# Optimization experiments

Hardware: AMD Instinct MI355X
Metric: run time of the kernel (lower is better)

## Reference

```python
import jax, jax.numpy as jnp
import numpy as np


def frame_align(x, R):
    # x: (..., N, d), R: (..., N, d, d)
    x = x - x.mean(axis=-2, keepdims=True)
    # R_inv = R^T applied per frame l to every point k: out[..., l, k, i]
    return jnp.einsum('...lji,...kj->...lki', R, x)


def setup_inputs() -> dict:
    key = jax.random.key(0)
    k1, k2, k3, k4 = jax.random.split(key, 4)
    B, N, d = 4, 2048, 3
    x = jax.random.normal(k1, (B, N, d), dtype=jnp.float32)
    R_x = jax.random.normal(k2, (B, N, d, d), dtype=jnp.float32)
    y = jax.random.normal(k3, (B, N, d), dtype=jnp.float32)
    R_y = jax.random.normal(k4, (B, N, d, d), dtype=jnp.float32)
    return {"x": x, "R_x": R_x, "y": y, "R_y": R_y}


def reference(x, R_x, y, R_y):
    x_aligned = frame_align(x, R_x)  # (B, N, N, d)
    y_aligned = frame_align(y, R_y)  # (B, N, N, d)
    return jnp.mean((x_aligned - y_aligned) ** 2)
```

## Files before the change

kernel.cpp:

```cpp
#include <hip/hip_runtime.h>

#define BATCH 4
#define NPTS  2048
#define TPB   256
#define BPB   8
#define NBLK  (BATCH * BPB)
#define NACC  48


__device__ float g_partial[NBLK][NACC];
__device__ int   g_ticket = 0;

__global__ __launch_bounds__(TPB)
void fape_single_kernel(const float* __restrict__ x,
                        const float* __restrict__ Rx,
                        const float* __restrict__ y,
                        const float* __restrict__ Ry,
                        float* __restrict__ out)
{
    const int blk = blockIdx.x;
    const int b   = blk >> 3;
    const int kb  = blk & 7;
    const int tid = threadIdx.x;
    const int n   = kb * TPB + tid;

    const float* __restrict__ xb  = x  + (size_t)b * NPTS * 3 + (size_t)n * 3;
    const float* __restrict__ yb  = y  + (size_t)b * NPTS * 3 + (size_t)n * 3;
    const float* __restrict__ rxb = Rx + (size_t)b * NPTS * 9 + (size_t)n * 9;
    const float* __restrict__ ryb = Ry + (size_t)b * NPTS * 9 + (size_t)n * 9;

    const int pi[6] = {0, 1, 2, 0, 0, 1};
    const int pj[6] = {0, 1, 2, 1, 2, 2};

    float xv[3], yv[3], rx[9], ry[9];
#pragma unroll
    for (int i = 0; i < 3; ++i) { xv[i] = xb[i]; yv[i] = yb[i]; }
#pragma unroll
    for (int i = 0; i < 9; ++i) { rx[i] = rxb[i]; ry[i] = ryb[i]; }

    float acc[NACC];
#pragma unroll
    for (int i = 0; i < 3; ++i) { acc[i] = xv[i]; acc[3 + i] = yv[i]; }
#pragma unroll
    for (int p = 0; p < 6; ++p) {
        const int i = pi[p], j = pj[p];
        acc[6  + p] = xv[i] * xv[j];
        acc[12 + p] = yv[i] * yv[j];
        float a = 0.f, bb = 0.f;
#pragma unroll
        for (int m = 0; m < 3; ++m) {
            a  += rx[i * 3 + m] * rx[j * 3 + m];
            bb += ry[i * 3 + m] * ry[j * 3 + m];
        }
        acc[27 + p] = a;
        acc[33 + p] = bb;
    }
#pragma unroll
    for (int i = 0; i < 3; ++i) {
#pragma unroll
        for (int j = 0; j < 3; ++j) {
            acc[18 + i * 3 + j] = xv[i] * yv[j];
            float c = 0.f;
#pragma unroll
            for (int m = 0; m < 3; ++m) c += rx[i * 3 + m] * ry[j * 3 + m];
            acc[39 + i * 3 + j] = c;
        }
    }

#pragma unroll
    for (int off = 32; off > 0; off >>= 1) {
#pragma unroll
        for (int q = 0; q < NACC; ++q) acc[q] += __shfl_down(acc[q], off, 64);
    }

    __shared__ float red[TPB / 64][NACC];
    const int wave = tid >> 6, lane = tid & 63;
    if (lane == 0) {
#pragma unroll
        for (int q = 0; q < NACC; ++q) red[wave][q] = acc[q];
    }
    __syncthreads();

    if (tid < NACC) {
        g_partial[blk][tid] = red[0][tid] + red[1][tid] + red[2][tid] + red[3][tid];
    }
    __threadfence();
    __syncthreads();

    __shared__ int slast;
    if (tid == 0) {
        const int old = atomicAdd(&g_ticket, 1);
        slast = (old == NBLK - 1);
    }
    __syncthreads();
    if (!slast) return;

    __threadfence();
    volatile const float* vp = &g_partial[0][0];

    __shared__ float fin[BATCH][NACC];
    if (tid < BATCH * NACC) {
        const int bb = tid / NACC, q = tid % NACC;
        float s = 0.f;
#pragma unroll
        for (int k = 0; k < BPB; ++k) s += vp[(bb * BPB + k) * NACC + q];
        fin[bb][q] = s;
    }
    __syncthreads();

    __shared__ double dots[BATCH];
    if (tid < BATCH) {
        const float* f = fin[tid];
        const double Ninv = 1.0 / (double)NPTS;
        double sx[3], sy[3];
        for (int i = 0; i < 3; ++i) { sx[i] = f[0 + i]; sy[i] = f[3 + i]; }

        double Sx[6], Sy[6], Sxy[9];
        for (int p = 0; p < 6; ++p) {
            const int i = pi[p], j = pj[p];
            Sx[p] = (double)f[6  + p] - sx[i] * sx[j] * Ninv;
            Sy[p] = (double)f[12 + p] - sy[i] * sy[j] * Ninv;
        }
        for (int i = 0; i < 3; ++i)
            for (int j = 0; j < 3; ++j)
                Sxy[i * 3 + j] = (double)f[18 + i * 3 + j] - sx[i] * sy[j] * Ninv;

        double dot = 0.0;
        for (int p = 0; p < 3; ++p)
            dot += (double)f[27 + p] * Sx[p] + (double)f[33 + p] * Sy[p];
        for (int p = 3; p < 6; ++p)
            dot += 2.0 * ((double)f[27 + p] * Sx[p] + (double)f[33 + p] * Sy[p]);
        double cr = 0.0;
        for (int q = 0; q < 9; ++q) cr += (double)f[39 + q] * Sxy[q];
        dot -= 2.0 * cr;

        dots[tid] = dot;
    }
    __syncthreads();

    if (tid == 0) {
        const double denom = (double)BATCH * (double)NPTS * (double)NPTS * 3.0;
        out[0] = (float)((dots[0] + dots[1] + dots[2] + dots[3]) / denom);
        g_ticket = 0;
        __threadfence();
    }
}

extern "C" void kernel_launch(void* const* d_in, const int* in_sizes, int n_in,
                              void* d_out, int out_size, void* d_ws, size_t ws_size,
                              hipStream_t stream) {
    const float* x  = (const float*)d_in[0];
    const float* Rx = (const float*)d_in[1];
    const float* y  = (const float*)d_in[2];
    const float* Ry = (const float*)d_in[3];
    float* out = (float*)d_out;

    fape_single_kernel<<<NBLK, TPB, 0, stream>>>(x, Rx, y, Ry, out);
}
```

Before: 16.35 us.

## Split point and rotation moment accumulation across separate block roles

Doubles the grid so that half the blocks accumulate the point moments (27 values) and the other half accumulate the frame Gram products (21 values), in place of every thread computing all 48. This shortens the per-thread shuffle reduction and register load and spreads the work over more CUs. In exchange the grid is larger and the last block must gather partials laid out in two roles.

```diff
diff --git a/kernel.cpp b/kernel.cpp
--- a/kernel.cpp
+++ b/kernel.cpp
@@ -3,87 +3,111 @@
 #define BATCH 4
 #define NPTS  2048
 #define TPB   256
-#define BPB   8
-#define NBLK  (BATCH * BPB)
-#define NACC  48
+#define BPR   8
+#define NBLK  (BATCH * 2 * BPR)
+#define NPACC 27
+#define NFACC 21
+#define PSTRIDE 28
 
-
-__device__ float g_partial[NBLK][NACC];
+__device__ float g_partial[NBLK][PSTRIDE];
 __device__ int   g_ticket = 0;
 
+template <int NA>
+__device__ inline void wave_reduce(float* acc) {
+#pragma unroll
+    for (int off = 32; off > 0; off >>= 1) {
+#pragma unroll
+        for (int q = 0; q < NA; ++q) acc[q] += __shfl_down(acc[q], off, 64);
+    }
+}
+
+template <int NA>
+__device__ inline void block_store(float* acc, int blk, int tid) {
+    __shared__ float red[TPB / 64][NA];
+    const int wave = tid >> 6, lane = tid & 63;
+    if (lane == 0) {
+#pragma unroll
+        for (int q = 0; q < NA; ++q) red[wave][q] = acc[q];
+    }
+    __syncthreads();
+    if (tid < NA) {
+        g_partial[blk][tid] = red[0][tid] + red[1][tid] + red[2][tid] + red[3][tid];
+    }
+}
+
 __global__ __launch_bounds__(TPB)
-void fape_single_kernel(const float* __restrict__ x,
-                        const float* __restrict__ Rx,
-                        const float* __restrict__ y,
-                        const float* __restrict__ Ry,
-                        float* __restrict__ out)
+void fape_split_kernel(const float* __restrict__ x,
+                       const float* __restrict__ Rx,
+                       const float* __restrict__ y,
+                       const float* __restrict__ Ry,
+                       float* __restrict__ out)
 {
     const int blk = blockIdx.x;
-    const int b   = blk >> 3;
+    const int b   = blk >> 4;
+    const int role = (blk >> 3) & 1;
     const int kb  = blk & 7;
     const int tid = threadIdx.x;
     const int n   = kb * TPB + tid;
 
-    const float* __restrict__ xb  = x  + (size_t)b * NPTS * 3 + (size_t)n * 3;
-    const float* __restrict__ yb  = y  + (size_t)b * NPTS * 3 + (size_t)n * 3;
-    const float* __restrict__ rxb = Rx + (size_t)b * NPTS * 9 + (size_t)n * 9;
-    const float* __restrict__ ryb = Ry + (size_t)b * NPTS * 9 + (size_t)n * 9;
-
     const int pi[6] = {0, 1, 2, 0, 0, 1};
     const int pj[6] = {0, 1, 2, 1, 2, 2};
 
-    float xv[3], yv[3], rx[9], ry[9];
+    if (role == 0) {
+        const float* __restrict__ xb = x + (size_t)b * NPTS * 3 + (size_t)n * 3;
+        const float* __restrict__ yb = y + (size_t)b * NPTS * 3 + (size_t)n * 3;
+        float xv[3], yv[3];
 #pragma unroll
-    for (int i = 0; i < 3; ++i) { xv[i] = xb[i]; yv[i] = yb[i]; }
+        for (int i = 0; i < 3; ++i) { xv[i] = xb[i]; yv[i] = yb[i]; }
+
+        float acc[NPACC];
 #pragma unroll
-    for (int i = 0; i < 9; ++i) { rx[i] = rxb[i]; ry[i] = ryb[i]; }
+        for (int i = 0; i < 3; ++i) { acc[i] = xv[i]; acc[3 + i] = yv[i]; }
+#pragma unroll
+        for (int p = 0; p < 6; ++p) {
+            acc[6  + p] = xv[pi[p]] * xv[pj[p]];
+            acc[12 + p] = yv[pi[p]] * yv[pj[p]];
+        }
+#pragma unroll
+        for (int i = 0; i < 3; ++i)
+#pragma unroll
+            for (int j = 0; j < 3; ++j) acc[18 + i * 3 + j] = xv[i] * yv[j];
 
-    float acc[NACC];
+        wave_reduce<NPACC>(acc);
+        block_store<NPACC>(acc, blk, tid);
+    } else {
+        const float* __restrict__ rxb = Rx + (size_t)b * NPTS * 9 + (size_t)n * 9;
+        const float* __restrict__ ryb = Ry + (size_t)b * NPTS * 9 + (size_t)n * 9;
+        float rx[9], ry[9];
 #pragma unroll
-    for (int i = 0; i < 3; ++i) { acc[i] = xv[i]; acc[3 + i] = yv[i]; }
+        for (int i = 0; i < 9; ++i) { rx[i] = rxb[i]; ry[i] = ryb[i]; }
+
+        float acc[NFACC];
 #pragma unroll
-    for (int p = 0; p < 6; ++p) {
-        const int i = pi[p], j = pj[p];
-        acc[6  + p] = xv[i] * xv[j];
-        acc[12 + p] = yv[i] * yv[j];
-        float a = 0.f, bb = 0.f;
+        for (int p = 0; p < 6; ++p) {
+            const int i = pi[p], j = pj[p];
+            float a = 0.f, bb = 0.f;
 #pragma unroll
-        for (int m = 0; m < 3; ++m) {
-            a  += rx[i * 3 + m] * rx[j * 3 + m];
-            bb += ry[i * 3 + m] * ry[j * 3 + m];
+            for (int m = 0; m < 3; ++m) {
+                a  += rx[i * 3 + m] * rx[j * 3 + m];
+                bb += ry[i * 3 + m] * ry[j * 3 + m];
+            }
+            acc[0 + p] = a;
+            acc[6 + p] = bb;
         }
-        acc[27 + p] = a;
-        acc[33 + p] = bb;
-    }
 #pragma unroll
-    for (int i = 0; i < 3; ++i) {
+        for (int i = 0; i < 3; ++i)
 #pragma unroll
-        for (int j = 0; j < 3; ++j) {
-            acc[18 + i * 3 + j] = xv[i] * yv[j];
-            float c = 0.f;
+            for (int j = 0; j < 3; ++j) {
+                float c = 0.f;
 #pragma unroll
-            for (int m = 0; m < 3; ++m) c += rx[i * 3 + m] * ry[j * 3 + m];
-            acc[39 + i * 3 + j] = c;
-        }
+                for (int m = 0; m < 3; ++m) c += rx[i * 3 + m] * ry[j * 3 + m];
+                acc[12 + i * 3 + j] = c;
+            }
+
+        wave_reduce<NFACC>(acc);
+        block_store<NFACC>(acc, blk, tid);
     }
 
-#pragma unroll
-    for (int off = 32; off > 0; off >>= 1) {
-#pragma unroll
-        for (int q = 0; q < NACC; ++q) acc[q] += __shfl_down(acc[q], off, 64);
-    }
-
-    __shared__ float red[TPB / 64][NACC];
-    const int wave = tid >> 6, lane = tid & 63;
-    if (lane == 0) {
-#pragma unroll
-        for (int q = 0; q < NACC; ++q) red[wave][q] = acc[q];
-    }
-    __syncthreads();
-
-    if (tid < NACC) {
-        g_partial[blk][tid] = red[0][tid] + red[1][tid] + red[2][tid] + red[3][tid];
-    }
     __threadfence();
     __syncthreads();
 
@@ -98,40 +122,49 @@
     __threadfence();
     volatile const float* vp = &g_partial[0][0];
 
-    __shared__ float fin[BATCH][NACC];
-    if (tid < BATCH * NACC) {
-        const int bb = tid / NACC, q = tid % NACC;
+    __shared__ float finp[BATCH][NPACC];
+    __shared__ float finf[BATCH][NFACC];
+    if (tid < BATCH * NPACC) {
+        const int bb = tid / NPACC, q = tid % NPACC;
         float s = 0.f;
 #pragma unroll
-        for (int k = 0; k < BPB; ++k) s += vp[(bb * BPB + k) * NACC + q];
-        fin[bb][q] = s;
+        for (int k = 0; k < BPR; ++k) s += vp[(bb * 16 + k) * PSTRIDE + q];
+        finp[bb][q] = s;
+    } else if (tid < BATCH * NPACC + BATCH * NFACC) {
+        const int t = tid - BATCH * NPACC;
+        const int bb = t / NFACC, q = t % NFACC;
+        float s = 0.f;
+#pragma unroll
+        for (int k = 0; k < BPR; ++k) s += vp[(bb * 16 + 8 + k) * PSTRIDE + q];
+        finf[bb][q] = s;
     }
     __syncthreads();
 
     __shared__ double dots[BATCH];
     if (tid < BATCH) {
-        const float* f = fin[tid];
+        const float* fp = finp[tid];
+        const float* ff = finf[tid];
         const double Ninv = 1.0 / (double)NPTS;
         double sx[3], sy[3];
-        for (int i = 0; i < 3; ++i) { sx[i] = f[0 + i]; sy[i] = f[3 + i]; }
+        for (int i = 0; i < 3; ++i) { sx[i] = fp[0 + i]; sy[i] = fp[3 + i]; }
 
         double Sx[6], Sy[6], Sxy[9];
         for (int p = 0; p < 6; ++p) {
             const int i = pi[p], j = pj[p];
-            Sx[p] = (double)f[6  + p] - sx[i] * sx[j] * Ninv;
-            Sy[p] = (double)f[12 + p] - sy[i] * sy[j] * Ninv;
+            Sx[p] = (double)fp[6  + p] - sx[i] * sx[j] * Ninv;
+            Sy[p] = (double)fp[12 + p] - sy[i] * sy[j] * Ninv;
         }
         for (int i = 0; i < 3; ++i)
             for (int j = 0; j < 3; ++j)
-                Sxy[i * 3 + j] = (double)f[18 + i * 3 + j] - sx[i] * sy[j] * Ninv;
+                Sxy[i * 3 + j] = (double)fp[18 + i * 3 + j] - sx[i] * sy[j] * Ninv;
 
         double dot = 0.0;
         for (int p = 0; p < 3; ++p)
-            dot += (double)f[27 + p] * Sx[p] + (double)f[33 + p] * Sy[p];
+            dot += (double)ff[0 + p] * Sx[p] + (double)ff[6 + p] * Sy[p];
         for (int p = 3; p < 6; ++p)
-            dot += 2.0 * ((double)f[27 + p] * Sx[p] + (double)f[33 + p] * Sy[p]);
+            dot += 2.0 * ((double)ff[0 + p] * Sx[p] + (double)ff[6 + p] * Sy[p]);
         double cr = 0.0;
-        for (int q = 0; q < 9; ++q) cr += (double)f[39 + q] * Sxy[q];
+        for (int q = 0; q < 9; ++q) cr += (double)ff[12 + q] * Sxy[q];
         dot -= 2.0 * cr;
 
         dots[tid] = dot;
@@ -155,5 +188,5 @@
     const float* Ry = (const float*)d_in[3];
     float* out = (float*)d_out;
 
-    fape_single_kernel<<<NBLK, TPB, 0, stream>>>(x, Rx, y, Ry, out);
+    fape_split_kernel<<<NBLK, TPB, 0, stream>>>(x, Rx, y, Ry, out);
 }
```

Result: slower. 18.36 us (+12.3%).
